# Optimization experiments

Measured on AMD Instinct MI355X. Metric: run time of the kernel, lower is better.

## Reference

```python
import jax, jax.numpy as jnp
from jax import lax
import numpy as np


def setup_inputs() -> dict:
    key = jax.random.key(0)
    kx, kw = jax.random.split(key)
    # Binary {0,1} activations: the module's int8-cast/XOR/AND trick is only
    # meaningful XNOR-popcount math for binary inputs.
    x = jax.random.randint(kx, (32, 256, 58, 58), 0, 2).astype(jnp.float32)
    weight = jax.random.normal(kw, (256, 256, 3, 3), dtype=jnp.float32)
    return {"x": x, "weight": weight}


def reference(x, weight):
    # XNORConv2d.forward, stride=1, padding=0 (forward never pads).
    B, C, H, W = x.shape
    O, _, kh, kw = weight.shape
    n = C * H * W  # note: alpha normalizes by INPUT size, as in the source
    N = kh * kw

    # alpha = sum_{c,kh,kw} |w| / n, one scalar per output filter  -> (O,)
    alpha = jnp.sum(jnp.abs(weight), axis=(1, 2, 3)) / n

    # Binarized weights: sign(w) >= 0 -> {0,1}
    bw = (weight >= 0).astype(x.dtype)

    dn = lax.conv_dimension_numbers(x.shape, weight.shape, ("NCHW", "OIHW", "NCHW"))
    conv = lambda a, f: lax.conv_general_dilated(
        a, f, window_strides=(1, 1), padding="VALID", dimension_numbers=dn
    )

    # XNOR match count per (b, o, y, x): S = #(p==f) over c,kh,kw
    #   = conv(p, f) + conv(1-p, 1-f)
    S = conv(x, bw) + conv(1.0 - x, 1.0 - bw)  # (B, O, H', W')

    # popcount per channel = 2*s_c - N; summed over channels -> 2*S - C*N
    res = 2.0 * S - jnp.asarray(C * N, dtype=x.dtype)

    return alpha[None, :, None, None] * res
```

## Files before the change

### kernel.cpp

```cpp
#include <hip/hip_runtime.h>
#include <stdint.h>


#define BATCH 32
#define C_IN 256
#define OCH 256
#define HIN 58
#define WIN2 58
#define HOUT 56
#define WOUT 56
#define TAPS 9
#define WWORDS 8
#define HWIN (HIN * WIN2)
#define HWOUT (HOUT * WOUT)
#define NPOS (BATCH * HWIN)
#define OGRP 32

#define BCNT_ACC(a, v) asm("v_bcnt_u32_b32 %0, %1, %0" : "+v"(a) : "v"(v))

__global__ __launch_bounds__(256) void pack_x_kernel(
    const float* __restrict__ x, uint32_t* __restrict__ xp)
{
    int t = blockIdx.x * 256 + threadIdx.x;
    int p  = t >> 2;
    int wp = t & 3;
    int b = p / HWIN;
    int r = p - b * HWIN;
    const float* xb = x + ((size_t)(b * C_IN + wp * 64)) * HWIN + r;
    uint32_t m0 = 0u, m1 = 0u;
    #pragma unroll
    for (int j = 0; j < 32; ++j) {
        float v0 = xb[(size_t)j * HWIN];
        float v1 = xb[(size_t)(j + 32) * HWIN];
        m0 |= (v0 > 0.5f ? 1u : 0u) << j;
        m1 |= (v1 > 0.5f ? 1u : 0u) << j;
    }
    *(uint2*)(xp + (size_t)p * WWORDS + wp * 2) = make_uint2(m0, m1);
}

__global__ __launch_bounds__(256) void pack_w_kernel(
    const float* __restrict__ wt, uint32_t* __restrict__ wq,
    float* __restrict__ sA, float* __restrict__ sB)
{
    int o = blockIdx.x;
    int c = threadIdx.x;
    const float* wb = wt + ((size_t)o * C_IN + c) * TAPS;
    float wv[TAPS];
    float s = 0.f;
    #pragma unroll
    for (int t = 0; t < TAPS; ++t) {
        wv[t] = wb[t];
        s += fabsf(wv[t]);
    }
    int wave = c >> 6, lane = c & 63;
    #pragma unroll
    for (int t = 0; t < TAPS; ++t) {
        unsigned long long m = __ballot(wv[t] >= 0.0f);
        if (lane == 0) {
            wq[((size_t)t * OCH + o) * WWORDS + wave * 2]     = (uint32_t)m;
            wq[((size_t)t * OCH + o) * WWORDS + wave * 2 + 1] = (uint32_t)(m >> 32);
        }
    }
    __shared__ float red[256];
    red[c] = s;
    __syncthreads();
    for (int off = 128; off > 0; off >>= 1) {
        if (c < off) red[c] += red[c + off];
        __syncthreads();
    }
    if (c == 0) {
        float alpha = red[0] / (float)(C_IN * HWIN);
        sA[o] = -2.0f * alpha;
        sB[o] = (float)(C_IN * TAPS) * alpha;
    }
}

__global__ __launch_bounds__(256, 8) void xnor_main_kernel(
    const uint32_t* __restrict__ xp, const uint32_t* __restrict__ wq,
    const float* __restrict__ sA, const float* __restrict__ sB,
    float* __restrict__ out)
{
    int obase = blockIdx.y * OGRP;

    int m = blockIdx.x * 256 + threadIdx.x;
    int b = m / HWOUT;
    int r = m - b * HWOUT;
    int oy = r / WOUT;
    int ox = r - oy * WOUT;

    const uint32_t* xrow = xp + (((size_t)b * HIN + oy) * WIN2 + ox) * WWORDS;

    uint32_t acc[OGRP];
    #pragma unroll
    for (int i = 0; i < OGRP; ++i) acc[i] = 0u;

    uint4 x0 = *(const uint4*)(xrow);
    uint4 x1 = *(const uint4*)(xrow + 4);

    #pragma unroll 1
    for (int tap = 0; tap < TAPS; ++tap) {
        int t2 = (tap < TAPS - 1) ? tap + 1 : TAPS - 1;
        int dy2 = t2 / 3;
        int dx2 = t2 - dy2 * 3;
        const uint32_t* nsrc = xrow + (size_t)(dy2 * WIN2 + dx2) * WWORDS;
        uint4 nx0 = *(const uint4*)(nsrc);
        uint4 nx1 = *(const uint4*)(nsrc + 4);

        const uint32_t* wt = wq + ((size_t)tap * OCH + obase) * WWORDS;
        #pragma unroll
        for (int oo = 0; oo < OGRP; ++oo) {
            uint4 wa  = *(const uint4*)(wt + oo * 8 + 0);
            uint4 wb2 = *(const uint4*)(wt + oo * 8 + 4);
            uint32_t t;
            t = wa.x  ^ x0.x; BCNT_ACC(acc[oo], t);
            t = wa.y  ^ x0.y; BCNT_ACC(acc[oo], t);
            t = wa.z  ^ x0.z; BCNT_ACC(acc[oo], t);
            t = wa.w  ^ x0.w; BCNT_ACC(acc[oo], t);
            t = wb2.x ^ x1.x; BCNT_ACC(acc[oo], t);
            t = wb2.y ^ x1.y; BCNT_ACC(acc[oo], t);
            t = wb2.z ^ x1.z; BCNT_ACC(acc[oo], t);
            t = wb2.w ^ x1.w; BCNT_ACC(acc[oo], t);
        }
        x0 = nx0; x1 = nx1;
    }

    size_t ob = ((size_t)b * OCH + obase) * HWOUT + (size_t)oy * WOUT + ox;
    #pragma unroll
    for (int oo = 0; oo < OGRP; ++oo) {
        float P = (float)acc[oo];
        int o0 = obase + oo;
        out[ob + (size_t)oo * HWOUT] = fmaf(sA[o0], P, sB[o0]);
    }
}

extern "C" void kernel_launch(void* const* d_in, const int* in_sizes, int n_in,
                              void* d_out, int out_size, void* d_ws, size_t ws_size,
                              hipStream_t stream)
{
    const float* x  = (const float*)d_in[0];
    const float* wt = (const float*)d_in[1];
    float* out = (float*)d_out;

    char* ws = (char*)d_ws;
    uint32_t* xp = (uint32_t*)ws;
    uint32_t* wq = (uint32_t*)(ws + 3444736);
    float*    sA = (float*)(ws + 3444736 + 73728);
    float*    sB = (float*)(ws + 3444736 + 73728 + 1024);

    pack_x_kernel<<<dim3(1682), dim3(256), 0, stream>>>(x, xp);

    pack_w_kernel<<<dim3(OCH), dim3(256), 0, stream>>>(wt, wq, sA, sB);

    xnor_main_kernel<<<dim3(392, 8), dim3(256), 0, stream>>>(xp, wq, sA, sB, out);
}
```

Measured before the change: 297.0 us.

## Keep weights in registers per lane, stream input rows, stage output in LDS

After: 302.8 us. About the same (+2.0%).

```diff
diff --git a/kernel.cpp b/kernel.cpp
--- a/kernel.cpp
+++ b/kernel.cpp
@@ -14,9 +14,11 @@
 #define HWIN (HIN * WIN2)
 #define HWOUT (HOUT * WOUT)
 #define NPOS (BATCH * HWIN)
-#define OGRP 32
 
-#define BCNT_ACC(a, v) asm("v_bcnt_u32_b32 %0, %1, %0" : "+v"(a) : "v"(v))
+typedef unsigned int u32x8 __attribute__((ext_vector_type(8)));
+
+#define BCNT0(v) asm("v_bcnt_u32_b32 %0, %1, %0" : "+v"(a0) : "v"(v))
+#define BCNT1(v) asm("v_bcnt_u32_b32 %0, %1, %0" : "+v"(a1) : "v"(v))
 
 __global__ __launch_bounds__(256) void pack_x_kernel(
     const float* __restrict__ x, uint32_t* __restrict__ xp)
@@ -57,8 +59,8 @@
     for (int t = 0; t < TAPS; ++t) {
         unsigned long long m = __ballot(wv[t] >= 0.0f);
         if (lane == 0) {
-            wq[((size_t)t * OCH + o) * WWORDS + wave * 2]     = (uint32_t)m;
-            wq[((size_t)t * OCH + o) * WWORDS + wave * 2 + 1] = (uint32_t)(m >> 32);
+            wq[(size_t)(t * 8 + wave * 2)     * OCH + o] = (uint32_t)m;
+            wq[(size_t)(t * 8 + wave * 2 + 1) * OCH + o] = (uint32_t)(m >> 32);
         }
     }
     __shared__ float red[256];
@@ -75,61 +77,92 @@
     }
 }
 
-__global__ __launch_bounds__(256, 8) void xnor_main_kernel(
+__global__ __launch_bounds__(256, 5) void xnor_main_kernel(
     const uint32_t* __restrict__ xp, const uint32_t* __restrict__ wq,
     const float* __restrict__ sA, const float* __restrict__ sB,
     float* __restrict__ out)
 {
-    int obase = blockIdx.y * OGRP;
+    __shared__ float olds[64 * 57];
 
-    int m = blockIdx.x * 256 + threadIdx.x;
-    int b = m / HWOUT;
-    int r = m - b * HWOUT;
-    int oy = r / WOUT;
-    int ox = r - oy * WOUT;
+    int rj = blockIdx.x;
+    int b  = rj / HOUT;
+    int oy = rj - b * HOUT;
+    int obase = blockIdx.y * 64;
+    int lane = threadIdx.x & 63;
+    int wv_id = __builtin_amdgcn_readfirstlane((int)(threadIdx.x >> 6));
+    int o = obase + lane;
 
-    const uint32_t* xrow = xp + (((size_t)b * HIN + oy) * WIN2 + ox) * WWORDS;
+    uint32_t wreg[72];
+    #pragma unroll
+    for (int i = 0; i < 72; ++i)
+        wreg[i] = wq[(size_t)i * OCH + o];
+    float sAv = sA[o];
+    float sBv = sB[o];
 
-    uint32_t acc[OGRP];
-    #pragma unroll
-    for (int i = 0; i < OGRP; ++i) acc[i] = 0u;
+    int ox0 = wv_id * 14;
 
-    uint4 x0 = *(const uint4*)(xrow);
-    uint4 x1 = *(const uint4*)(xrow + 4);
+    const uint32_t* r0 = xp + (((size_t)b * HIN + oy + 0) * WIN2 + ox0) * WWORDS;
+    const uint32_t* r1 = xp + (((size_t)b * HIN + oy + 1) * WIN2 + ox0) * WWORDS;
+    const uint32_t* r2 = xp + (((size_t)b * HIN + oy + 2) * WIN2 + ox0) * WWORDS;
+
+    u32x8 W0a = *(const u32x8*)(r0);
+    u32x8 W0b = *(const u32x8*)(r0 + 8);
+    u32x8 W0c = *(const u32x8*)(r0 + 16);
+    u32x8 W1a = *(const u32x8*)(r1);
+    u32x8 W1b = *(const u32x8*)(r1 + 8);
+    u32x8 W1c = *(const u32x8*)(r1 + 16);
+    u32x8 W2a = *(const u32x8*)(r2);
+    u32x8 W2b = *(const u32x8*)(r2 + 8);
+    u32x8 W2c = *(const u32x8*)(r2 + 16);
 
     #pragma unroll 1
-    for (int tap = 0; tap < TAPS; ++tap) {
-        int t2 = (tap < TAPS - 1) ? tap + 1 : TAPS - 1;
-        int dy2 = t2 / 3;
-        int dx2 = t2 - dy2 * 3;
-        const uint32_t* nsrc = xrow + (size_t)(dy2 * WIN2 + dx2) * WWORDS;
-        uint4 nx0 = *(const uint4*)(nsrc);
-        uint4 nx1 = *(const uint4*)(nsrc + 4);
+    for (int i = 0; i < 14; ++i) {
+        uint32_t a0 = 0u, a1 = 0u, t;
+        #pragma unroll
+        for (int k = 0; k < 8; ++k) { t = W0a[k] ^ wreg[0 * 8 + k]; BCNT0(t); }
+        #pragma unroll
+        for (int k = 0; k < 8; ++k) { t = W0b[k] ^ wreg[1 * 8 + k]; BCNT1(t); }
+        #pragma unroll
+        for (int k = 0; k < 8; ++k) { t = W0c[k] ^ wreg[2 * 8 + k]; BCNT0(t); }
+        r0 += 8;
+        W0a = *(const u32x8*)(r0);
+        W0b = *(const u32x8*)(r0 + 8);
+        W0c = *(const u32x8*)(r0 + 16);
+        #pragma unroll
+        for (int k = 0; k < 8; ++k) { t = W1a[k] ^ wreg[3 * 8 + k]; BCNT1(t); }
+        #pragma unroll
+        for (int k = 0; k < 8; ++k) { t = W1b[k] ^ wreg[4 * 8 + k]; BCNT0(t); }
+        #pragma unroll
+        for (int k = 0; k < 8; ++k) { t = W1c[k] ^ wreg[5 * 8 + k]; BCNT1(t); }
+        r1 += 8;
+        W1a = *(const u32x8*)(r1);
+        W1b = *(const u32x8*)(r1 + 8);
+        W1c = *(const u32x8*)(r1 + 16);
+        #pragma unroll
+        for (int k = 0; k < 8; ++k) { t = W2a[k] ^ wreg[6 * 8 + k]; BCNT0(t); }
+        #pragma unroll
+        for (int k = 0; k < 8; ++k) { t = W2b[k] ^ wreg[7 * 8 + k]; BCNT1(t); }
+        #pragma unroll
+        for (int k = 0; k < 8; ++k) { t = W2c[k] ^ wreg[8 * 8 + k]; BCNT0(t); }
+        r2 += 8;
+        W2a = *(const u32x8*)(r2);
+        W2b = *(const u32x8*)(r2 + 8);
+        W2c = *(const u32x8*)(r2 + 16);
 
-        const uint32_t* wt = wq + ((size_t)tap * OCH + obase) * WWORDS;
-        #pragma unroll
-        for (int oo = 0; oo < OGRP; ++oo) {
-            uint4 wa  = *(const uint4*)(wt + oo * 8 + 0);
-            uint4 wb2 = *(const uint4*)(wt + oo * 8 + 4);
-            uint32_t t;
-            t = wa.x  ^ x0.x; BCNT_ACC(acc[oo], t);
-            t = wa.y  ^ x0.y; BCNT_ACC(acc[oo], t);
-            t = wa.z  ^ x0.z; BCNT_ACC(acc[oo], t);
-            t = wa.w  ^ x0.w; BCNT_ACC(acc[oo], t);
-            t = wb2.x ^ x1.x; BCNT_ACC(acc[oo], t);
-            t = wb2.y ^ x1.y; BCNT_ACC(acc[oo], t);
-            t = wb2.z ^ x1.z; BCNT_ACC(acc[oo], t);
-            t = wb2.w ^ x1.w; BCNT_ACC(acc[oo], t);
-        }
-        x0 = nx0; x1 = nx1;
+        float P = (float)(a0 + a1);
+        olds[lane * 57 + (ox0 + i)] = fmaf(sAv, P, sBv);
     }
 
-    size_t ob = ((size_t)b * OCH + obase) * HWOUT + (size_t)oy * WOUT + ox;
-    #pragma unroll
-    for (int oo = 0; oo < OGRP; ++oo) {
-        float P = (float)acc[oo];
-        int o0 = obase + oo;
-        out[ob + (size_t)oo * HWOUT] = fmaf(sA[o0], P, sB[o0]);
+    __syncthreads();
+
+    size_t obb = ((size_t)b * OCH + obase) * HWOUT + (size_t)oy * WOUT;
+    int tau = threadIdx.x;
+    #pragma unroll 1
+    for (int i = 0; i < 14; ++i) {
+        int flat = i * 256 + tau;
+        int op = flat / 56;
+        int pp = flat - op * 56;
+        out[obb + (size_t)op * HWOUT + pp] = olds[op * 57 + pp];
     }
 }
 
@@ -151,5 +184,5 @@
 
     pack_w_kernel<<<dim3(OCH), dim3(256), 0, stream>>>(wt, wq, sA, sB);
 
-    xnor_main_kernel<<<dim3(392, 8), dim3(256), 0, stream>>>(xp, wq, sA, sB, out);
+    xnor_main_kernel<<<dim3(1792, 4), dim3(256), 0, stream>>>(xp, wq, sA, sB, out);
 }
```

## Replace XNOR-popcount loop with int8 MFMA over ±1 expanded activations

Applied to the files above, without the earlier changes.

Result: faster. 285.3 us (-3.9%).

```diff
diff --git a/kernel.cpp b/kernel.cpp
--- a/kernel.cpp
+++ b/kernel.cpp
@@ -14,9 +14,17 @@
 #define HWIN (HIN * WIN2)
 #define HWOUT (HOUT * WOUT)
 #define NPOS (BATCH * HWIN)
-#define OGRP 32
-
-#define BCNT_ACC(a, v) asm("v_bcnt_u32_b32 %0, %1, %0" : "+v"(a) : "v"(v))
+
+#define AP 144
+#define NAPOS 232
+#define BCH 8192
+
+typedef int   i32x4  __attribute__((ext_vector_type(4)));
+typedef int   i32x16 __attribute__((ext_vector_type(16)));
+typedef float f32x4  __attribute__((ext_vector_type(4)));
+
+#define MFMA(acc, va, vb) \
+    asm volatile("v_mfma_i32_32x32x32_i8 %0, %1, %2, %0" : "+v"(acc) : "v"(va), "v"(vb))
 
 __global__ __launch_bounds__(256) void pack_x_kernel(
     const float* __restrict__ x, uint32_t* __restrict__ xp)
@@ -38,29 +46,24 @@
     *(uint2*)(xp + (size_t)p * WWORDS + wp * 2) = make_uint2(m0, m1);
 }
 
-__global__ __launch_bounds__(256) void pack_w_kernel(
-    const float* __restrict__ wt, uint32_t* __restrict__ wq,
-    float* __restrict__ sA, float* __restrict__ sB)
+__global__ __launch_bounds__(256) void pack_w8_kernel(
+    const float* __restrict__ wt, char* __restrict__ wq8, float* __restrict__ sA)
 {
     int o = blockIdx.x;
     int c = threadIdx.x;
     const float* wb = wt + ((size_t)o * C_IN + c) * TAPS;
-    float wv[TAPS];
     float s = 0.f;
+    char sg[TAPS];
     #pragma unroll
     for (int t = 0; t < TAPS; ++t) {
-        wv[t] = wb[t];
-        s += fabsf(wv[t]);
-    }
-    int wave = c >> 6, lane = c & 63;
-    #pragma unroll
-    for (int t = 0; t < TAPS; ++t) {
-        unsigned long long m = __ballot(wv[t] >= 0.0f);
-        if (lane == 0) {
-            wq[((size_t)t * OCH + o) * WWORDS + wave * 2]     = (uint32_t)m;
-            wq[((size_t)t * OCH + o) * WWORDS + wave * 2 + 1] = (uint32_t)(m >> 32);
-        }
-    }
+        float v = wb[t];
+        s += fabsf(v);
+        sg[t] = (v >= 0.0f) ? (char)1 : (char)-1;
+    }
+    #pragma unroll
+    for (int t = 0; t < TAPS; ++t)
+        wq8[(size_t)o * (TAPS * C_IN) + t * C_IN + c] = sg[t];
+
     __shared__ float red[256];
     red[c] = s;
     __syncthreads();
@@ -68,69 +71,150 @@
         if (c < off) red[c] += red[c + off];
         __syncthreads();
     }
-    if (c == 0) {
-        float alpha = red[0] / (float)(C_IN * HWIN);
-        sA[o] = -2.0f * alpha;
-        sB[o] = (float)(C_IN * TAPS) * alpha;
-    }
-}
-
-__global__ __launch_bounds__(256, 8) void xnor_main_kernel(
-    const uint32_t* __restrict__ xp, const uint32_t* __restrict__ wq,
-    const float* __restrict__ sA, const float* __restrict__ sB,
-    float* __restrict__ out)
-{
-    int obase = blockIdx.y * OGRP;
-
-    int m = blockIdx.x * 256 + threadIdx.x;
-    int b = m / HWOUT;
-    int r = m - b * HWOUT;
-    int oy = r / WOUT;
-    int ox = r - oy * WOUT;
-
-    const uint32_t* xrow = xp + (((size_t)b * HIN + oy) * WIN2 + ox) * WWORDS;
-
-    uint32_t acc[OGRP];
-    #pragma unroll
-    for (int i = 0; i < OGRP; ++i) acc[i] = 0u;
-
-    uint4 x0 = *(const uint4*)(xrow);
-    uint4 x1 = *(const uint4*)(xrow + 4);
-
-    #pragma unroll 1
-    for (int tap = 0; tap < TAPS; ++tap) {
-        int t2 = (tap < TAPS - 1) ? tap + 1 : TAPS - 1;
-        int dy2 = t2 / 3;
-        int dx2 = t2 - dy2 * 3;
-        const uint32_t* nsrc = xrow + (size_t)(dy2 * WIN2 + dx2) * WWORDS;
-        uint4 nx0 = *(const uint4*)(nsrc);
-        uint4 nx1 = *(const uint4*)(nsrc + 4);
-
-        const uint32_t* wt = wq + ((size_t)tap * OCH + obase) * WWORDS;
-        #pragma unroll
-        for (int oo = 0; oo < OGRP; ++oo) {
-            uint4 wa  = *(const uint4*)(wt + oo * 8 + 0);
-            uint4 wb2 = *(const uint4*)(wt + oo * 8 + 4);
-            uint32_t t;
-            t = wa.x  ^ x0.x; BCNT_ACC(acc[oo], t);
-            t = wa.y  ^ x0.y; BCNT_ACC(acc[oo], t);
-            t = wa.z  ^ x0.z; BCNT_ACC(acc[oo], t);
-            t = wa.w  ^ x0.w; BCNT_ACC(acc[oo], t);
-            t = wb2.x ^ x1.x; BCNT_ACC(acc[oo], t);
-            t = wb2.y ^ x1.y; BCNT_ACC(acc[oo], t);
-            t = wb2.z ^ x1.z; BCNT_ACC(acc[oo], t);
-            t = wb2.w ^ x1.w; BCNT_ACC(acc[oo], t);
+    if (c == 0) sA[o] = red[0] / (float)(C_IN * HWIN);
+}
+
+__global__ __launch_bounds__(512)
+__attribute__((amdgpu_waves_per_eu(4, 4)))
+void xnor_mfma_kernel(
+    const uint32_t* __restrict__ xp, const char* __restrict__ wq8,
+    const float* __restrict__ sA, float* __restrict__ out)
+{
+    __shared__ __attribute__((aligned(16))) char lds[NAPOS * AP + 2 * BCH];
+    char* Alds = lds;
+    char* Blds = lds + NAPOS * AP;
+    float* Cbuf = (float*)lds;
+
+    int blk = blockIdx.x;
+    int b   = blk / 28;
+    int rp  = blk - b * 28;
+    int oy0 = rp * 2;
+    int tid  = threadIdx.x;
+    int wv   = tid >> 6;
+    int lane = tid & 63;
+    int l31  = lane & 31;
+    int e    = lane >> 5;
+    int mgrp = wv & 1;
+    int ngrp = wv >> 1;
+
+    int baseA[2];
+    #pragma unroll
+    for (int mi = 0; mi < 2; ++mi) {
+        int p = (mgrp * 2 + mi) * 32 + l31;
+        int r = (p * 586) >> 15;
+        int c = p - 56 * r;
+        baseA[mi] = (r * 58 + c) * AP + e * 16;
+    }
+    int bofsB = (ngrp * 64 + l31) * 32 + e * 16;
+    float al0 = sA[ngrp * 64 + l31];
+    float al1 = sA[ngrp * 64 + 32 + l31];
+
+    i32x16 acc00 = {0}, acc01 = {0}, acc10 = {0}, acc11 = {0};
+    asm volatile("" : "+v"(acc00), "+v"(acc01), "+v"(acc10), "+v"(acc11));
+    asm volatile("s_nop 7\n\ts_nop 7");
+
+#define STAGE_A(KH)                                                        \
+    {                                                                      \
+        _Pragma("unroll")                                                  \
+        for (int ir = 0; ir < 4; ++ir) {                                   \
+            if (tid < 464) {                                               \
+                int iw = tid >> 3, c16 = tid & 7;                          \
+                uint32_t wvx = xp[((size_t)(b * HIN + oy0 + ir) * WIN2 + iw) * WWORDS \
+                                  + (KH) * 4 + (c16 >> 1)];                \
+                uint32_t bits = (c16 & 1) ? (wvx >> 16) : (wvx & 0xFFFFu); \
+                i32x4 v;                                                   \
+                _Pragma("unroll")                                          \
+                for (int d = 0; d < 4; ++d) {                              \
+                    uint32_t n  = (bits >> (4 * d)) & 0xFu;                \
+                    uint32_t sp = (n * 0x204081u) & 0x01010101u;           \
+                    v[d] = (int)~(sp * 0xFEu);                             \
+                }                                                          \
+                *(i32x4*)(Alds + (ir * 58 + iw) * AP + c16 * 16) = v;      \
+            }                                                              \
+        }                                                                  \
+    }
+
+    STAGE_A(0);
+
+    const char* wqt = wq8 + (size_t)(tid >> 1) * (TAPS * C_IN) + (tid & 1) * 16;
+    char* bw = Blds + ((tid >> 1) * 32 + (tid & 1) * 16);
+    i32x4 regP = *(const i32x4*)(wqt + 0);
+    *(i32x4*)(bw + 0) = regP;
+    regP = *(const i32x4*)(wqt + 32);
+    __syncthreads();
+
+    #pragma unroll
+    for (int s = 0; s < 72; ++s) {
+        if (s == 36) { STAGE_A(1); __syncthreads(); }
+        const int kh  = s / 36;
+        const int tap = (s - kh * 36) >> 2;
+        const int kb  = s & 3;
+        const int dy  = tap / 3, dx = tap - dy * 3;
+        const int s2   = (s + 2 > 71) ? 71 : s + 2;
+        const int kh2  = s2 / 36;
+        const int tap2 = (s2 - kh2 * 36) >> 2;
+        const int kb2  = s2 & 3;
+        i32x4 regN = *(const i32x4*)(wqt + tap2 * 256 + kh2 * 128 + kb2 * 32);
+
+        const int ka = (dy * 58 + dx) * AP + kb * 32;
+        const char* Br = Blds + (s & 1) * BCH;
+        i32x4 a0 = *(const i32x4*)(Alds + baseA[0] + ka);
+        i32x4 a1 = *(const i32x4*)(Alds + baseA[1] + ka);
+        i32x4 b0 = *(const i32x4*)(Br + bofsB);
+        i32x4 b1 = *(const i32x4*)(Br + bofsB + 1024);
+        MFMA(acc00, a0, b0);
+        MFMA(acc01, a0, b1);
+        MFMA(acc10, a1, b0);
+        MFMA(acc11, a1, b1);
+
+        *(i32x4*)(bw + ((s & 1) ^ 1) * BCH) = regP;
+        regP = regN;
+        __syncthreads();
+    }
+
+    asm volatile("s_nop 7\n\ts_nop 7");
+
+    size_t ob = ((size_t)b * OCH) * HWOUT + (size_t)oy0 * WOUT;
+    #pragma unroll
+    for (int q = 0; q < 4; ++q) {
+        __syncthreads();
+        if (mgrp == (q >> 1)) {
+            const int mi = q & 1;
+            #pragma unroll
+            for (int ni = 0; ni < 2; ++ni) {
+                float al = ni ? al1 : al0;
+                int o = ngrp * 64 + ni * 32 + l31;
+                i32x16 A;
+                if (mi == 0 && ni == 0) A = acc00;
+                else if (mi == 0)       A = acc01;
+                else if (ni == 0)       A = acc10;
+                else                    A = acc11;
+                #pragma unroll
+                for (int g = 0; g < 4; ++g) {
+                    f32x4 vv;
+                    vv[0] = al * (float)A[4 * g + 0];
+                    vv[1] = al * (float)A[4 * g + 1];
+                    vv[2] = al * (float)A[4 * g + 2];
+                    vv[3] = al * (float)A[4 * g + 3];
+                    int pl = g * 8 + 4 * e;
+                    *(f32x4*)(Cbuf + (size_t)o * 36 + pl) = vv;
+                }
+            }
         }
-        x0 = nx0; x1 = nx1;
-    }
-
-    size_t ob = ((size_t)b * OCH + obase) * HWOUT + (size_t)oy * WOUT + ox;
-    #pragma unroll
-    for (int oo = 0; oo < OGRP; ++oo) {
-        float P = (float)acc[oo];
-        int o0 = obase + oo;
-        out[ob + (size_t)oo * HWOUT] = fmaf(sA[o0], P, sB[o0]);
-    }
+        __syncthreads();
+        #pragma unroll 1
+        for (int i = 0; i < 16; ++i) {
+            int idx = i * 512 + tid;
+            int o = idx >> 5, pl = idx & 31;
+            int pg = q * 32 + pl;
+            if (pg < 112) {
+                int r = (pg >= 56) ? 1 : 0;
+                int c = pg - 56 * r;
+                out[ob + (size_t)o * HWOUT + r * WOUT + c] = Cbuf[o * 36 + pl];
+            }
+        }
+    }
+#undef STAGE_A
 }
 
 extern "C" void kernel_launch(void* const* d_in, const int* in_sizes, int n_in,
@@ -142,14 +226,13 @@
     float* out = (float*)d_out;
 
     char* ws = (char*)d_ws;
-    uint32_t* xp = (uint32_t*)ws;
-    uint32_t* wq = (uint32_t*)(ws + 3444736);
-    float*    sA = (float*)(ws + 3444736 + 73728);
-    float*    sB = (float*)(ws + 3444736 + 73728 + 1024);
+    uint32_t* xp  = (uint32_t*)ws;
+    char*     wq8 = (char*)(ws + 3444736);
+    float*    sAp = (float*)(ws + 3444736 + 589824);
 
     pack_x_kernel<<<dim3(1682), dim3(256), 0, stream>>>(x, xp);
 
-    pack_w_kernel<<<dim3(OCH), dim3(256), 0, stream>>>(wt, wq, sA, sB);
-
-    xnor_main_kernel<<<dim3(392, 8), dim3(256), 0, stream>>>(xp, wq, sA, sB, out);
-}
+    pack_w8_kernel<<<dim3(OCH), dim3(256), 0, stream>>>(wt, wq8, sAp);
+
+    xnor_mfma_kernel<<<dim3(896), dim3(512), 0, stream>>>(xp, wq8, sAp, out);
+}
```
